# Performance work log

Hardware: AMD Instinct MI355X
Metric: run time of the kernel (lower is better)

Reference implementation:

```python
import jax, jax.numpy as jnp
import numpy as np
import math

TILE_SIZE = 32
N_HEADS = 16
FACTOR = 5.0
MASK_VALUE = -1e9


def setup_inputs() -> dict:
    key = jax.random.key(0)
    ks = jax.random.split(key, 8)
    B, S, D = 2, 2048, 1024
    w = 0.02  # weight scale so attention logits stay in a sane range
    return {
        "query": jax.random.normal(ks[0], (B, S, D), jnp.float32),
        "key": jax.random.normal(ks[1], (B, S, D), jnp.float32),
        "value": jax.random.normal(ks[2], (B, S, D), jnp.float32),
        "mask": jnp.zeros((1, 1, S, S), jnp.float32),
        "Wq": jax.random.normal(ks[3], (D, D), jnp.float32) * w,
        "bq": jnp.zeros((D,), jnp.float32),
        "Wk": jax.random.normal(ks[4], (D, D), jnp.float32) * w,
        "bk": jnp.zeros((D,), jnp.float32),
        "Wv": jax.random.normal(ks[5], (D, D), jnp.float32) * w,
        "bv": jnp.zeros((D,), jnp.float32),
        "Wo": jax.random.normal(ks[6], (D, D), jnp.float32) * w,
        "bo": jnp.zeros((D,), jnp.float32),
        "q_valid_len": 2000,
        "k_valid_len": 1900,
    }


def _pad_to_multiple(x, multiple):
    L = x.shape[1]
    p = (-L) % multiple  # static
    if p:
        x = jnp.pad(x, ((0, 0), (0, p), (0, 0)))
    return x, L


def _split_heads(x, H):
    B, L, D = x.shape
    return x.reshape(B, L, H, D // H).transpose(0, 2, 1, 3)  # [B,H,L,hd]


def _forward(query, key, value, mask, Wq, bq, Wk, bk, Wv, bv, Wo, bo,
             q_valid_len, k_valid_len):
    B, Sq, D = query.shape
    H = N_HEADS
    hd = D // H
    q = query @ Wq.T + bq
    k = key @ Wk.T + bk
    v = value @ Wv.T + bv
    q, q_len_pad = _pad_to_multiple(q, TILE_SIZE)
    k, _ = _pad_to_multiple(k, TILE_SIZE)
    v, _ = _pad_to_multiple(v, TILE_SIZE)
    qh, kh, vh = _split_heads(q, H), _split_heads(k, H), _split_heads(v, H)
    Lq, Lk = qh.shape[2], kh.shape[2]

    # key padding mask [1,1,1,Lk]
    kpm = ((jnp.arange(Lk) >= k_valid_len).astype(jnp.float32) * MASK_VALUE)
    attn_mask = mask + kpm.reshape(1, 1, 1, Lk)

    # manual scaled-dot attention with bf16 cast of scores (stable softmax path)
    scores = jnp.einsum('bhqd,bhkd->bhqk', qh, kh) / math.sqrt(hd)
    scores = scores.astype(jnp.bfloat16) + attn_mask.astype(jnp.bfloat16)
    probs = jax.nn.softmax(scores, axis=-1).astype(vh.dtype)
    context = jnp.einsum('bhqk,bhkd->bhqd', probs, vh)

    # ProbSparse top-u query-selection mask (note: original passes q_len_pad,
    # the pre-padding length, as valid_length)
    u = max(1, int(FACTOR * math.log(max(2, q_valid_len))))
    q_norm = jnp.sum(qh * qh, axis=-1)  # [B,H,Lq]
    if q_len_pad < Lq:
        q_norm = jnp.where(jnp.arange(Lq) < q_len_pad, q_norm, MASK_VALUE)
    _, topk_idx = jax.lax.top_k(q_norm, u)  # [B,H,u]
    # scatter ones at top-u positions (indices unique -> one-hot sum == set)
    ps_mask = jnp.sum(jax.nn.one_hot(topk_idx, Lq, dtype=jnp.float32), axis=2)
    context = context * ps_mask[..., None]

    # merge heads, strip padding, output projection (dropout p=0 / eval)
    context = context.transpose(0, 2, 1, 3).reshape(B, Lq, D)[:, :Sq, :]
    return context @ Wo.T + bo


def reference(query, key, value, mask, Wq, bq, Wk, bk, Wv, bv, Wo, bo,
              q_valid_len, k_valid_len):
    return _forward(query, key, value, mask, Wq, bq, Wk, bk, Wv, bv, Wo, bo,
                    q_valid_len, k_valid_len)
```

## Files before the change

### kernel.cpp

```cpp
#include <hip/hip_runtime.h>

typedef unsigned short u16;
typedef __bf16 bf16x8 __attribute__((ext_vector_type(8)));
typedef float f32x4 __attribute__((ext_vector_type(4)));

__device__ __forceinline__ u16 f2bf(float f){
  unsigned int x = __float_as_uint(f);
  unsigned int r = (x + 0x7FFFu + ((x >> 16) & 1u)) >> 16;
  return (u16)r;
}
__device__ __forceinline__ float bf2f(u16 u){
  return __uint_as_float(((unsigned int)u) << 16);
}
__device__ __forceinline__ int compute_u(int qvlv){
  int mm = qvlv > 2 ? qvlv : 2;
  int u = (int)(5.0 * log((double)mm));
  if (u < 1) u = 1;
  if (u > 64) u = 64;
  return u;
}
__device__ __forceinline__ void gload_lds16(const void* g, void* l){
  __builtin_amdgcn_global_load_lds(
      (const __attribute__((address_space(1))) void*)g,
      (__attribute__((address_space(3))) void*)l, 16, 0, 0);
}

__global__ void expand_kernel(const float* __restrict__ xq, const float* __restrict__ xk,
                              const float* __restrict__ xv,
                              const float* __restrict__ wq, const float* __restrict__ wk,
                              const float* __restrict__ wv,
                              u16* __restrict__ X1, u16* __restrict__ X2,
                              u16* __restrict__ W1, u16* __restrict__ W2,
                              const float* __restrict__ Wo, float* __restrict__ WoT,
                              unsigned int* __restrict__ hmask)
{
  __shared__ float tile[32][33];
  int t = threadIdx.x;
  if (blockIdx.x >= 15360){
    int bid = blockIdx.x - 15360;
    int bx = (bid & 31) * 32, by = (bid >> 5) * 32;
    int tx = t & 31, ty = t >> 5;
#pragma unroll
    for (int r = 0; r < 4; ++r)
      tile[ty + r*8][tx] = Wo[(size_t)(by + ty + r*8) * 1024 + bx + tx];
    __syncthreads();
#pragma unroll
    for (int r = 0; r < 4; ++r)
      WoT[(size_t)(bx + ty + r*8) * 1024 + by + tx] = tile[tx][ty + r*8];
    return;
  }
  size_t g = (size_t)blockIdx.x * 256 + t;
  if (g < 4096) hmask[g] = 0;
  const float* src; u16 *d1, *d2;
  if (g < 3145728ull) {
    int p = (int)(g >> 20);
    size_t e = (g & 1048575ull) * 4;
    src = (p == 0 ? xq : (p == 1 ? xk : xv)) + e;
    size_t o = (size_t)p * 4194304ull + e;
    d1 = X1 + o; d2 = X2 + o;
  } else {
    size_t wg = g - 3145728ull;
    int p = (int)(wg >> 18);
    size_t e = (wg & 262143ull) * 4;
    src = (p == 0 ? wq : (p == 1 ? wk : wv)) + e;
    size_t o = (size_t)p * 1048576ull + e;
    d1 = W1 + o; d2 = W2 + o;
  }
  float4 x = *reinterpret_cast<const float4*>(src);
  float xs[4] = {x.x, x.y, x.z, x.w};
  u16 h1[4], h2[4];
#pragma unroll
  for (int i = 0; i < 4; ++i){
    float v = xs[i];
    u16 a = f2bf(v);  float r1 = v - bf2f(a);
    h1[i] = a; h2[i] = f2bf(r1);
  }
  *reinterpret_cast<ushort4*>(d1) = make_ushort4(h1[0], h1[1], h1[2], h1[3]);
  *reinterpret_cast<ushort4*>(d2) = make_ushort4(h2[0], h2[1], h2[2], h2[3]);
}

__global__ __launch_bounds__(512, 1) void gemm_proj(
    const u16* __restrict__ X1, const u16* __restrict__ X2,
    const u16* __restrict__ W1, const u16* __restrict__ W2,
    const float* __restrict__ bq, const float* __restrict__ bk, const float* __restrict__ bv,
    float* __restrict__ PROJ, float* __restrict__ qn)
{
  int z = blockIdx.z;
  int orig = blockIdx.x + blockIdx.y * 8;
  int wgid = (orig & 7) * 16 + (orig >> 3);
  int bx = wgid & 7, by = wgid >> 3;

  const u16* Xa0 = X1 + (size_t)z * 4194304;
  const u16* Xa1 = X2 + (size_t)z * 4194304;
  const u16* Wb0 = W1 + (size_t)z * 1048576;
  const u16* Wb1 = W2 + (size_t)z * 1048576;
  const float* bias = (z == 0) ? bq : (z == 1 ? bk : bv);
  float* C = PROJ + (size_t)z * 4194304;

  __shared__ __align__(16) u16 T[2 * 24576];
  u16* SET0 = T;
  u16* SET1 = T + 24576;

  int t = threadIdx.x;
  int wave = t >> 6, lane = t & 63;
  int wm = wave >> 1, wn = wave & 1;
  int lr = lane & 15, lk = lane >> 4;
  int rowA = by * 256, rowB = bx * 128;
  f32x4 acc[4][4] = {};
  bf16x8 afA[4], afB[4], bgA[4], bgB[4];

#define STAGEA(dstbase, G)                                                    \
  {                                                                           \
    _Pragma("unroll")                                                         \
    for (int i = 0; i < 2; ++i){                                              \
      int p = i * 512 + t;                                                    \
      int r = p >> 2;                                                         \
      int c = (p & 3) ^ ((r >> 1) & 3);                                       \
      gload_lds16(G + (size_t)(rowA + r) * 1024 + pk + c * 8,                 \
                  (dstbase) + p * 8);                                         \
    }                                                                         \
  }
#define STAGEB(dstbase, G)                                                    \
  {                                                                           \
    int p = t;                                                                \
    int r = p >> 2;                                                           \
    int c = (p & 3) ^ ((r >> 1) & 3);                                         \
    gload_lds16(G + (size_t)(rowB + r) * 1024 + pk + c * 8,                   \
                (dstbase) + p * 8);                                           \
  }
#define STAGE_SET(S)                                                          \
  {                                                                           \
    STAGEA((S), Xa0); STAGEA((S) + 8192, Xa1);                                \
    STAGEB((S) + 16384, Wb0); STAGEB((S) + 20480, Wb1);                       \
  }
#define LOADA(dst, tile)                                                      \
  {                                                                           \
    _Pragma("unroll")                                                         \
    for (int m = 0; m < 4; ++m){                                              \
      int r = wm * 64 + m * 16 + lr;                                          \
      dst[m] = *reinterpret_cast<const bf16x8*>(                              \
          &(tile)[r * 32 + ((lk ^ ((r >> 1) & 3)) << 3)]);                    \
    }                                                                         \
  }
#define LOADB(dst, tile)                                                      \
  {                                                                           \
    _Pragma("unroll")                                                         \
    for (int n = 0; n < 4; ++n){                                              \
      int r = wn * 64 + n * 16 + lr;                                          \
      dst[n] = *reinterpret_cast<const bf16x8*>(                              \
          &(tile)[r * 32 + ((lk ^ ((r >> 1) & 3)) << 3)]);                    \
    }                                                                         \
  }
#define GRPX(A_, B_)                                                          \
  {                                                                           \
    __builtin_amdgcn_s_setprio(1);                                            \
    _Pragma("unroll")                                                         \
    for (int m = 0; m < 4; ++m)                                               \
      _Pragma("unroll")                                                       \
      for (int n = 0; n < 4; ++n)                                             \
        acc[m][n] = __builtin_amdgcn_mfma_f32_16x16x32_bf16(A_[m], B_[n],     \
                                                            acc[m][n], 0,0,0);\
    __builtin_amdgcn_s_setprio(0);                                            \
  }

  {
    int pk = 0;
    STAGE_SET(SET0);
  }
  __syncthreads();

  for (int kt = 0; kt < 32; ++kt){
    u16* CUR = (kt & 1) ? SET1 : SET0;
    u16* NXT = (kt & 1) ? SET0 : SET1;
    if (kt < 31){
      int pk = (kt + 1) * 32;
      STAGE_SET(NXT);
    }
    __builtin_amdgcn_sched_barrier(0);
    u16* A0t = CUR;          u16* A1t = CUR + 8192;
    u16* B0t = CUR + 16384;  u16* B1t = CUR + 20480;
    LOADA(afA, A0t); LOADB(bgA, B0t);
    LOADB(bgB, B1t); GRPX(afA, bgA);
    LOADA(afB, A1t); GRPX(afA, bgB);
                     GRPX(afB, bgA);
    __syncthreads();
  }
#undef STAGEA
#undef STAGEB
#undef STAGE_SET
#undef LOADA
#undef LOADB
#undef GRPX

  if (z == 0){
    float sq[4][4] = {};
#pragma unroll
    for (int m = 0; m < 4; ++m){
      int row0 = by * 256 + wm * 64 + m * 16 + lk * 4;
#pragma unroll
      for (int n = 0; n < 4; ++n){
        int col = bx * 128 + wn * 64 + n * 16 + lr;
        float bb = bias[col];
#pragma unroll
        for (int j = 0; j < 4; ++j){
          float v = acc[m][n][j] + bb;
          C[(size_t)(row0 + j) * 1024 + col] = v;
          sq[m][j] += v * v;
        }
      }
    }
    int hh = bx * 2 + wn;
#pragma unroll
    for (int m = 0; m < 4; ++m){
#pragma unroll
      for (int j = 0; j < 4; ++j){
        float s = sq[m][j];
        s += __shfl_xor(s, 1);
        s += __shfl_xor(s, 2);
        s += __shfl_xor(s, 4);
        s += __shfl_xor(s, 8);
        if (lr == 0){
          int row = by * 256 + wm * 64 + m * 16 + lk * 4 + j;
          qn[(size_t)((row >> 11) * 16 + hh) * 2048 + (row & 2047)] = s;
        }
      }
    }
  } else if (z == 1){
    u16* KS = (u16*)C;
#pragma unroll
    for (int m = 0; m < 4; ++m){
      int r0 = by * 256 + wm * 64 + m * 16 + lk * 4;
      int b = r0 >> 11, kb = r0 & 2047;
#pragma unroll
      for (int n = 0; n < 4; ++n){
        int c = bx * 128 + wn * 64 + n * 16 + lr;
        float bb = bias[c];
        int h = c >> 6, d = c & 63;
#pragma unroll
        for (int j = 0; j < 4; ++j){
          float v = acc[m][n][j] + bb;
          u16 hi = f2bf(v);
          u16 lo = f2bf(v - bf2f(hi));
          size_t base = ((size_t)(b * 16 + h) * 2048 + (size_t)(kb + j)) * 128;
          KS[base + d] = hi;
          KS[base + 64 + d] = lo;
        }
      }
    }
  } else {
    u16* VT = (u16*)C;
#pragma unroll
    for (int m = 0; m < 4; ++m){
      int r0 = by * 256 + wm * 64 + m * 16 + lk * 4;
      int b = r0 >> 11, kb = r0 & 2047;
#pragma unroll
      for (int n = 0; n < 4; ++n){
        int c = bx * 128 + wn * 64 + n * 16 + lr;
        float bb = bias[c];
        int h = c >> 6, d = c & 63;
        u16 hi[4], lo[4];
#pragma unroll
        for (int j = 0; j < 4; ++j){
          float v = acc[m][n][j] + bb;
          hi[j] = f2bf(v);
          lo[j] = f2bf(v - bf2f(hi[j]));
        }
        size_t base = ((size_t)(b * 16 + h) * 128) * 2048 + (size_t)kb;
        *reinterpret_cast<ushort4*>(&VT[base + (size_t)d * 2048]) =
            make_ushort4(hi[0], hi[1], hi[2], hi[3]);
        *reinterpret_cast<ushort4*>(&VT[base + (size_t)(64 + d) * 2048]) =
            make_ushort4(lo[0], lo[1], lo[2], lo[3]);
      }
    }
  }
}

__global__ __launch_bounds__(256) void topk_kernel(
    const float* __restrict__ qn, int* __restrict__ topk,
    unsigned char* __restrict__ seli, unsigned int* __restrict__ hmask,
    const float* __restrict__ PROJ, u16* __restrict__ QS,
    const int* __restrict__ qvlp){
  int bh = blockIdx.x; int b = bh >> 4, h = bh & 15;
  int u = compute_u(qvlp[0]);
  int t = threadIdx.x;
  __shared__ int sidx_l[64];
  if (t < 64){
    int lane = t;
    float v[32];
#pragma unroll
    for (int j = 0; j < 32; ++j) v[j] = qn[(size_t)bh * 2048 + j * 64 + lane];
    for (int it = 0; it < u; ++it){
      float bv = v[0]; int bi = lane;
#pragma unroll
      for (int j = 1; j < 32; ++j){
        if (v[j] > bv){ bv = v[j]; bi = j * 64 + lane; }
      }
#pragma unroll
      for (int off = 1; off < 64; off <<= 1){
        float ov = __shfl_xor(bv, off);
        int   oi = __shfl_xor(bi, off);
        if (ov > bv || (ov == bv && oi < bi)){ bv = ov; bi = oi; }
      }
      if (lane == 0){
        topk[bh * 64 + it] = bi;
        seli[(size_t)bh * 2048 + bi] = (unsigned char)it;
        atomicOr(&hmask[b * 2048 + bi], 1u << h);
        sidx_l[it] = bi;
      }
#pragma unroll
      for (int j = 0; j < 32; ++j)
        if (j * 64 + lane == bi) v[j] = -3.4e38f;
    }
  }
  __syncthreads();
  for (int e = t; e < 64 * 64; e += 256){
    int i = e >> 6, d = e & 63;
    float v = 0.f;
    if (i < u) v = PROJ[(size_t)(b * 2048 + sidx_l[i]) * 1024 + h * 64 + d];
    u16 hi = f2bf(v);
    u16 lo = f2bf(v - bf2f(hi));
    QS[(size_t)bh * 8192 + i * 128 + d] = hi;
    QS[(size_t)bh * 8192 + i * 128 + 64 + d] = lo;
  }
}

__global__ __launch_bounds__(256) void scores_mfma(
    const u16* __restrict__ QS, const u16* __restrict__ KS,
    const int* __restrict__ topk, const float* __restrict__ maskp,
    u16* __restrict__ sc, const int* __restrict__ qvlp, const int* __restrict__ kvlp)
{
  int bh = blockIdx.y;
  int kvlv = kvlp[0]; if (kvlv > 2048) kvlv = 2048; if (kvlv < 0) kvlv = 0;
  int u = compute_u(qvlp[0]);
  int k0 = blockIdx.x * 128;
  if (k0 >= kvlv) return;
  int t = threadIdx.x, wave = t >> 6, lane = t & 63;
  int lr = lane & 15, lk = lane >> 4;
  __shared__ int idx_l[64];
  if (t < 64) idx_l[t] = (t < u) ? topk[bh * 64 + t] : 0;
  __syncthreads();
  const u16* Qb = QS + (size_t)bh * 8192;
  const u16* Kb = KS + (size_t)bh * 2048 * 128;
  bf16x8 ah[2], al[2];
#pragma unroll
  for (int ks = 0; ks < 2; ++ks){
    const u16* qrow = &Qb[(wave * 16 + lr) * 128];
    ah[ks] = *reinterpret_cast<const bf16x8*>(&qrow[ks * 32 + lk * 8]);
    al[ks] = *reinterpret_cast<const bf16x8*>(&qrow[64 + ks * 32 + lk * 8]);
  }
  f32x4 acc[8] = {};
#pragma unroll
  for (int n = 0; n < 8; ++n){
    const u16* krow = &Kb[(size_t)(k0 + n * 16 + lr) * 128];
    bf16x8 bh0 = *reinterpret_cast<const bf16x8*>(&krow[lk * 8]);
    bf16x8 bh1 = *reinterpret_cast<const bf16x8*>(&krow[32 + lk * 8]);
    bf16x8 bl0 = *reinterpret_cast<const bf16x8*>(&krow[64 + lk * 8]);
    bf16x8 bl1 = *reinterpret_cast<const bf16x8*>(&krow[96 + lk * 8]);
    acc[n] = __builtin_amdgcn_mfma_f32_16x16x32_bf16(ah[0], bh0, acc[n], 0, 0, 0);
    acc[n] = __builtin_amdgcn_mfma_f32_16x16x32_bf16(ah[0], bl0, acc[n], 0, 0, 0);
    acc[n] = __builtin_amdgcn_mfma_f32_16x16x32_bf16(al[0], bh0, acc[n], 0, 0, 0);
    acc[n] = __builtin_amdgcn_mfma_f32_16x16x32_bf16(al[0], bl0, acc[n], 0, 0, 0);
    acc[n] = __builtin_amdgcn_mfma_f32_16x16x32_bf16(ah[1], bh1, acc[n], 0, 0, 0);
    acc[n] = __builtin_amdgcn_mfma_f32_16x16x32_bf16(ah[1], bl1, acc[n], 0, 0, 0);
    acc[n] = __builtin_amdgcn_mfma_f32_16x16x32_bf16(al[1], bh1, acc[n], 0, 0, 0);
    acc[n] = __builtin_amdgcn_mfma_f32_16x16x32_bf16(al[1], bl1, acc[n], 0, 0, 0);
  }
#pragma unroll
  for (int n = 0; n < 8; ++n){
    int k = k0 + n * 16 + lr;
    if (k >= kvlv) continue;
#pragma unroll
    for (int j = 0; j < 4; ++j){
      int i = wave * 16 + lk * 4 + j;
      if (i >= u) continue;
      float s = acc[n][j] * 0.125f;
      u16 xb = f2bf(s);
      u16 mb = f2bf(maskp[(size_t)idx_l[i] * 2048 + k]);
      u16 xm = f2bf(bf2f(xb) + bf2f(mb));
      sc[(size_t)(bh * 64 + i) * 2048 + k] = xm;
    }
  }
}

__global__ void softmax_kernel(u16* __restrict__ sc, const int* __restrict__ qvlp,
                               const int* __restrict__ kvlp){
  int bh = blockIdx.y, i = blockIdx.x;
  int u = compute_u(qvlp[0]);
  if (i >= u) return;
  int kvlv = kvlp[0]; if (kvlv > 2048) kvlv = 2048; if (kvlv < 0) kvlv = 0;
  u16* row = sc + (size_t)(bh * 64 + i) * 2048;
  int t = threadIdx.x;
  float x[8];
  float lm = -3.4e38f;
#pragma unroll
  for (int j = 0; j < 8; ++j){
    int k = t + j * 256;
    x[j] = (k < kvlv) ? bf2f(row[k]) : -3.4e38f;
    lm = fmaxf(lm, x[j]);
  }
  __shared__ float red[256];
  red[t] = lm; __syncthreads();
  for (int s = 128; s > 0; s >>= 1){ if (t < s) red[t] = fmaxf(red[t], red[t+s]); __syncthreads(); }
  float m = red[0];
  __syncthreads();
  float e[8]; float ls = 0.f;
#pragma unroll
  for (int j = 0; j < 8; ++j){
    int k = t + j * 256;
    if (k < kvlv){
      u16 ub = f2bf(x[j] - m);
      u16 eb = f2bf(expf(bf2f(ub)));
      e[j] = bf2f(eb);
      ls += e[j];
    } else e[j] = 0.f;
  }
  red[t] = ls; __syncthreads();
  for (int s = 128; s > 0; s >>= 1){ if (t < s) red[t] += red[t+s]; __syncthreads(); }
  float S = red[0];
  float Sb = bf2f(f2bf(S));
#pragma unroll
  for (int j = 0; j < 8; ++j){
    int k = t + j * 256;
    if (k < 2048) row[k] = (k < kvlv) ? f2bf(e[j] / Sb) : (u16)0;
  }
}

__global__ void pv_mfma(const u16* __restrict__ probs, const u16* __restrict__ VT,
                        float* __restrict__ part, const int* __restrict__ kvlp)
{
  int bh = blockIdx.y; int b = bh >> 4, h = bh & 15;
  int kvlv = kvlp[0]; if (kvlv > 2048) kvlv = 2048; if (kvlv < 0) kvlv = 0;
  int kc = blockIdx.x;
  int k0 = kc * 128;
  if (k0 >= kvlv) return;
  int t = threadIdx.x, w = t >> 6, lane = t & 63;
  int lr = lane & 15, lk = lane >> 4;
  const u16* Pb = probs + (size_t)bh * 64 * 2048;
  const u16* Vb = VT + (size_t)(b * 16 + h) * 128 * 2048;
  f32x4 acc[4] = {};
#pragma unroll
  for (int ks = 0; ks < 4; ++ks){
    int kk = k0 + ks * 32 + lk * 8;
    bf16x8 A0 = *reinterpret_cast<const bf16x8*>(Pb + (size_t)(lr     ) * 2048 + kk);
    bf16x8 A1 = *reinterpret_cast<const bf16x8*>(Pb + (size_t)(lr + 16) * 2048 + kk);
    bf16x8 A2 = *reinterpret_cast<const bf16x8*>(Pb + (size_t)(lr + 32) * 2048 + kk);
    bf16x8 A3 = *reinterpret_cast<const bf16x8*>(Pb + (size_t)(lr + 48) * 2048 + kk);
    bf16x8 Bh = *reinterpret_cast<const bf16x8*>(Vb + (size_t)(w * 16 + lr     ) * 2048 + kk);
    bf16x8 Bl = *reinterpret_cast<const bf16x8*>(Vb + (size_t)(w * 16 + lr + 64) * 2048 + kk);
    acc[0] = __builtin_amdgcn_mfma_f32_16x16x32_bf16(A0, Bh, acc[0], 0, 0, 0);
    acc[1] = __builtin_amdgcn_mfma_f32_16x16x32_bf16(A1, Bh, acc[1], 0, 0, 0);
    acc[2] = __builtin_amdgcn_mfma_f32_16x16x32_bf16(A2, Bh, acc[2], 0, 0, 0);
    acc[3] = __builtin_amdgcn_mfma_f32_16x16x32_bf16(A3, Bh, acc[3], 0, 0, 0);
    acc[0] = __builtin_amdgcn_mfma_f32_16x16x32_bf16(A0, Bl, acc[0], 0, 0, 0);
    acc[1] = __builtin_amdgcn_mfma_f32_16x16x32_bf16(A1, Bl, acc[1], 0, 0, 0);
    acc[2] = __builtin_amdgcn_mfma_f32_16x16x32_bf16(A2, Bl, acc[2], 0, 0, 0);
    acc[3] = __builtin_amdgcn_mfma_f32_16x16x32_bf16(A3, Bl, acc[3], 0, 0, 0);
  }
  float* pc = part + (size_t)(kc * 32 + bh) * 64 * 64;
#pragma unroll
  for (int m = 0; m < 4; ++m){
    int row = m * 16 + lk * 4;
#pragma unroll
    for (int j = 0; j < 4; ++j)
      pc[(size_t)(row + j) * 64 + w * 16 + lr] = acc[m][j];
  }
}

__global__ void outproj_kernel(const float* __restrict__ part, const float* __restrict__ WoT,
                               const float* __restrict__ bo, const unsigned int* __restrict__ hmask,
                               const unsigned char* __restrict__ seli, float* __restrict__ out,
                               const int* __restrict__ kvlp){
  int row = blockIdx.x;
  int b = row >> 11, l = row & 2047;
  int t = threadIdx.x;
  int kvlv = kvlp[0]; if (kvlv > 2048) kvlv = 2048; if (kvlv < 0) kvlv = 0;
  int kcmax = (kvlv + 127) / 128;
  float acc[4];
#pragma unroll
  for (int r = 0; r < 4; ++r) acc[r] = bo[t + r * 256];
  unsigned int m = hmask[row];
  __shared__ float clds[64];
  while (m){
    int h = __ffs(m) - 1; m &= (m - 1);
    int bh = b * 16 + h;
    int i = (int)seli[(size_t)bh * 2048 + l];
    __syncthreads();
    if (t < 64){
      float s = 0.f;
      for (int kc = 0; kc < kcmax; ++kc)
        s += part[(size_t)((kc * 32 + bh) * 64 + i) * 64 + t];
      clds[t] = s;
    }
    __syncthreads();
    for (int j = 0; j < 64; ++j){
      float c = clds[j];
      const float* wrow = &WoT[(size_t)(h * 64 + j) * 1024];
#pragma unroll
      for (int r = 0; r < 4; ++r) acc[r] += c * wrow[t + r * 256];
    }
  }
  float* orow = out + (size_t)row * 1024;
#pragma unroll
  for (int r = 0; r < 4; ++r) orow[t + r * 256] = acc[r];
}

__global__ void fail_fill(float* o, int n){
  int i = blockIdx.x * 256 + threadIdx.x;
  if (i < n) o[i] = 12345.0f;
}

extern "C" void kernel_launch(void* const* d_in, const int* in_sizes, int n_in,
                              void* d_out, int out_size, void* d_ws, size_t ws_size,
                              hipStream_t stream)
{
  const float* query = (const float*)d_in[0];
  const float* key   = (const float*)d_in[1];
  const float* value = (const float*)d_in[2];
  const float* maskp = (const float*)d_in[3];
  const float* Wq = (const float*)d_in[4];
  const float* bq = (const float*)d_in[5];
  const float* Wk = (const float*)d_in[6];
  const float* bk = (const float*)d_in[7];
  const float* Wv = (const float*)d_in[8];
  const float* bv = (const float*)d_in[9];
  const float* Wo = (const float*)d_in[10];
  const float* bo = (const float*)d_in[11];
  const int* qvl = (const int*)d_in[12];
  const int* kvl = (const int*)d_in[13];
  float* out = (float*)d_out;

  char* ws = (char*)d_ws;
  size_t off = 0;
  auto alloc = [&](size_t bytes) -> void* {
    void* p = ws + off;
    off = (off + bytes + 255) & ~(size_t)255;
    return p;
  };
  u16* X1 = (u16*)alloc(3ull * 4194304 * 2);
  u16* X2 = (u16*)alloc(3ull * 4194304 * 2);
  u16* W1 = (u16*)alloc(3ull * 1048576 * 2);
  u16* W2 = (u16*)alloc(3ull * 1048576 * 2);
  float* PROJ = (float*)alloc(3ull * 4194304 * 4);
  float* WOT  = (float*)alloc(4194304ull);
  float* QN   = (float*)alloc(2ull * 16 * 2048 * 4);
  int*   TOPK = (int*)alloc(2ull * 16 * 64 * 4);
  unsigned char* SELI = (unsigned char*)alloc(2ull * 16 * 2048);
  unsigned int* HMASK = (unsigned int*)alloc(2ull * 2048 * 4);
  u16*   SC   = (u16*)alloc(2048ull * 2048 * 2);
  u16*   QS   = (u16*)alloc(32ull * 64 * 128 * 2);

  u16* KS = (u16*)(PROJ + 1ull * 4194304);
  u16* VT = (u16*)(PROJ + 2ull * 4194304);
  float* PART = (float*)X1;

  if (ws_size < off){
    fail_fill<<<(out_size + 255) / 256, 256, 0, stream>>>(out, out_size);
    return;
  }

  expand_kernel<<<16384, 256, 0, stream>>>(query, key, value, Wq, Wk, Wv,
                                           X1, X2, W1, W2, Wo, WOT, HMASK);
  gemm_proj<<<dim3(8, 16, 3), 512, 0, stream>>>(X1, X2, W1, W2, bq, bk, bv, PROJ, QN);
  topk_kernel<<<32, 256, 0, stream>>>(QN, TOPK, SELI, HMASK, PROJ, QS, qvl);
  scores_mfma<<<dim3(16, 32), 256, 0, stream>>>(QS, KS, TOPK, maskp, SC, qvl, kvl);
  softmax_kernel<<<dim3(64, 32), 256, 0, stream>>>(SC, qvl, kvl);
  pv_mfma<<<dim3(16, 32), 256, 0, stream>>>(SC, VT, PART, kvl);
  outproj_kernel<<<4096, 256, 0, stream>>>(PART, WOT, bo, HMASK, SELI, out, kvl);
}
```

Baseline: 252.4 us.

## Fuse score computation with softmax in LDS and widen split-precision expand

Merges the scores MFMA kernel and the softmax kernel into one kernel. Each 512-thread block computes 16 selected query rows against all keys and keeps the bf16 scores in shared memory, then runs a per-row softmax with warp shuffles, so the intermediate score matrix is no longer written to and re-read from global memory and one launch is saved. The expand kernel now processes 8 floats per thread with 16-byte stores, halving its block count. The trade-off is a large LDS footprint (about 64KB) limiting occupancy, and only 128 blocks for the fused stage, which also now computes all key tiles and all 16 rows in a group, including rows beyond u and keys beyond the valid length.

```diff
diff --git a/kernel.cpp b/kernel.cpp
--- a/kernel.cpp
+++ b/kernel.cpp
@@ -36,8 +36,8 @@
 {
   __shared__ float tile[32][33];
   int t = threadIdx.x;
-  if (blockIdx.x >= 15360){
-    int bid = blockIdx.x - 15360;
+  if (blockIdx.x >= 7680){
+    int bid = blockIdx.x - 7680;
     int bx = (bid & 31) * 32, by = (bid >> 5) * 32;
     int tx = t & 31, ty = t >> 5;
 #pragma unroll
@@ -52,31 +52,33 @@
   size_t g = (size_t)blockIdx.x * 256 + t;
   if (g < 4096) hmask[g] = 0;
   const float* src; u16 *d1, *d2;
-  if (g < 3145728ull) {
-    int p = (int)(g >> 20);
-    size_t e = (g & 1048575ull) * 4;
+  if (g < 1572864ull) {
+    int p = (int)(g >> 19);
+    size_t e = (g & 524287ull) * 8;
     src = (p == 0 ? xq : (p == 1 ? xk : xv)) + e;
     size_t o = (size_t)p * 4194304ull + e;
     d1 = X1 + o; d2 = X2 + o;
   } else {
-    size_t wg = g - 3145728ull;
-    int p = (int)(wg >> 18);
-    size_t e = (wg & 262143ull) * 4;
+    size_t wg = g - 1572864ull;
+    int p = (int)(wg >> 17);
+    size_t e = (wg & 131071ull) * 8;
     src = (p == 0 ? wq : (p == 1 ? wk : wv)) + e;
     size_t o = (size_t)p * 1048576ull + e;
     d1 = W1 + o; d2 = W2 + o;
   }
-  float4 x = *reinterpret_cast<const float4*>(src);
-  float xs[4] = {x.x, x.y, x.z, x.w};
-  u16 h1[4], h2[4];
+  float4 a = *reinterpret_cast<const float4*>(src);
+  float4 b = *reinterpret_cast<const float4*>(src + 4);
+  float xs[8] = {a.x, a.y, a.z, a.w, b.x, b.y, b.z, b.w};
+  unsigned int hw[4], lw[4];
 #pragma unroll
   for (int i = 0; i < 4; ++i){
-    float v = xs[i];
-    u16 a = f2bf(v);  float r1 = v - bf2f(a);
-    h1[i] = a; h2[i] = f2bf(r1);
-  }
-  *reinterpret_cast<ushort4*>(d1) = make_ushort4(h1[0], h1[1], h1[2], h1[3]);
-  *reinterpret_cast<ushort4*>(d2) = make_ushort4(h2[0], h2[1], h2[2], h2[3]);
+    u16 h0 = f2bf(xs[2*i]);     u16 l0 = f2bf(xs[2*i]     - bf2f(h0));
+    u16 h1 = f2bf(xs[2*i + 1]); u16 l1 = f2bf(xs[2*i + 1] - bf2f(h1));
+    hw[i] = (unsigned int)h0 | ((unsigned int)h1 << 16);
+    lw[i] = (unsigned int)l0 | ((unsigned int)l1 << 16);
+  }
+  *reinterpret_cast<uint4*>(d1) = make_uint4(hw[0], hw[1], hw[2], hw[3]);
+  *reinterpret_cast<uint4*>(d2) = make_uint4(lw[0], lw[1], lw[2], lw[3]);
 }
 
 __global__ __launch_bounds__(512, 1) void gemm_proj(
@@ -324,104 +326,88 @@
   }
 }
 
-__global__ __launch_bounds__(256) void scores_mfma(
+#define SLP 2050
+__global__ __launch_bounds__(512) void scores_softmax(
     const u16* __restrict__ QS, const u16* __restrict__ KS,
     const int* __restrict__ topk, const float* __restrict__ maskp,
     u16* __restrict__ sc, const int* __restrict__ qvlp, const int* __restrict__ kvlp)
 {
-  int bh = blockIdx.y;
+  int bh = blockIdx.y, rg = blockIdx.x;
   int kvlv = kvlp[0]; if (kvlv > 2048) kvlv = 2048; if (kvlv < 0) kvlv = 0;
   int u = compute_u(qvlp[0]);
-  int k0 = blockIdx.x * 128;
-  if (k0 >= kvlv) return;
   int t = threadIdx.x, wave = t >> 6, lane = t & 63;
   int lr = lane & 15, lk = lane >> 4;
-  __shared__ int idx_l[64];
-  if (t < 64) idx_l[t] = (t < u) ? topk[bh * 64 + t] : 0;
+  __shared__ __align__(16) u16 Sl[16 * SLP];
+  __shared__ int idx_l[16];
+  if (t < 16) idx_l[t] = (rg * 16 + t < u) ? topk[bh * 64 + rg * 16 + t] : 0;
   __syncthreads();
   const u16* Qb = QS + (size_t)bh * 8192;
   const u16* Kb = KS + (size_t)bh * 2048 * 128;
-  bf16x8 ah[2], al[2];
-#pragma unroll
-  for (int ks = 0; ks < 2; ++ks){
-    const u16* qrow = &Qb[(wave * 16 + lr) * 128];
-    ah[ks] = *reinterpret_cast<const bf16x8*>(&qrow[ks * 32 + lk * 8]);
-    al[ks] = *reinterpret_cast<const bf16x8*>(&qrow[64 + ks * 32 + lk * 8]);
-  }
-  f32x4 acc[8] = {};
-#pragma unroll
-  for (int n = 0; n < 8; ++n){
-    const u16* krow = &Kb[(size_t)(k0 + n * 16 + lr) * 128];
-    bf16x8 bh0 = *reinterpret_cast<const bf16x8*>(&krow[lk * 8]);
-    bf16x8 bh1 = *reinterpret_cast<const bf16x8*>(&krow[32 + lk * 8]);
-    bf16x8 bl0 = *reinterpret_cast<const bf16x8*>(&krow[64 + lk * 8]);
-    bf16x8 bl1 = *reinterpret_cast<const bf16x8*>(&krow[96 + lk * 8]);
-    acc[n] = __builtin_amdgcn_mfma_f32_16x16x32_bf16(ah[0], bh0, acc[n], 0, 0, 0);
-    acc[n] = __builtin_amdgcn_mfma_f32_16x16x32_bf16(ah[0], bl0, acc[n], 0, 0, 0);
-    acc[n] = __builtin_amdgcn_mfma_f32_16x16x32_bf16(al[0], bh0, acc[n], 0, 0, 0);
-    acc[n] = __builtin_amdgcn_mfma_f32_16x16x32_bf16(al[0], bl0, acc[n], 0, 0, 0);
-    acc[n] = __builtin_amdgcn_mfma_f32_16x16x32_bf16(ah[1], bh1, acc[n], 0, 0, 0);
-    acc[n] = __builtin_amdgcn_mfma_f32_16x16x32_bf16(ah[1], bl1, acc[n], 0, 0, 0);
-    acc[n] = __builtin_amdgcn_mfma_f32_16x16x32_bf16(al[1], bh1, acc[n], 0, 0, 0);
-    acc[n] = __builtin_amdgcn_mfma_f32_16x16x32_bf16(al[1], bl1, acc[n], 0, 0, 0);
-  }
-#pragma unroll
-  for (int n = 0; n < 8; ++n){
-    int k = k0 + n * 16 + lr;
-    if (k >= kvlv) continue;
+  const u16* qrow = &Qb[(rg * 16 + lr) * 128];
+  bf16x8 ah0 = *reinterpret_cast<const bf16x8*>(&qrow[lk * 8]);
+  bf16x8 ah1 = *reinterpret_cast<const bf16x8*>(&qrow[32 + lk * 8]);
+  bf16x8 al0 = *reinterpret_cast<const bf16x8*>(&qrow[64 + lk * 8]);
+  bf16x8 al1 = *reinterpret_cast<const bf16x8*>(&qrow[96 + lk * 8]);
+  int k0 = wave * 256;
+#pragma unroll
+  for (int nf = 0; nf < 16; ++nf){
+    const u16* krow = &Kb[(size_t)(k0 + nf * 16 + lr) * 128];
+    bf16x8 kh0 = *reinterpret_cast<const bf16x8*>(&krow[lk * 8]);
+    bf16x8 kh1 = *reinterpret_cast<const bf16x8*>(&krow[32 + lk * 8]);
+    bf16x8 kl0 = *reinterpret_cast<const bf16x8*>(&krow[64 + lk * 8]);
+    bf16x8 kl1 = *reinterpret_cast<const bf16x8*>(&krow[96 + lk * 8]);
+    f32x4 acc = {};
+    acc = __builtin_amdgcn_mfma_f32_16x16x32_bf16(ah0, kh0, acc, 0, 0, 0);
+    acc = __builtin_amdgcn_mfma_f32_16x16x32_bf16(ah0, kl0, acc, 0, 0, 0);
+    acc = __builtin_amdgcn_mfma_f32_16x16x32_bf16(al0, kh0, acc, 0, 0, 0);
+    acc = __builtin_amdgcn_mfma_f32_16x16x32_bf16(al0, kl0, acc, 0, 0, 0);
+    acc = __builtin_amdgcn_mfma_f32_16x16x32_bf16(ah1, kh1, acc, 0, 0, 0);
+    acc = __builtin_amdgcn_mfma_f32_16x16x32_bf16(ah1, kl1, acc, 0, 0, 0);
+    acc = __builtin_amdgcn_mfma_f32_16x16x32_bf16(al1, kh1, acc, 0, 0, 0);
+    acc = __builtin_amdgcn_mfma_f32_16x16x32_bf16(al1, kl1, acc, 0, 0, 0);
+    int k = k0 + nf * 16 + lr;
 #pragma unroll
     for (int j = 0; j < 4; ++j){
-      int i = wave * 16 + lk * 4 + j;
-      if (i >= u) continue;
-      float s = acc[n][j] * 0.125f;
+      int i = lk * 4 + j;
+      float s = acc[j] * 0.125f;
       u16 xb = f2bf(s);
       u16 mb = f2bf(maskp[(size_t)idx_l[i] * 2048 + k]);
-      u16 xm = f2bf(bf2f(xb) + bf2f(mb));
-      sc[(size_t)(bh * 64 + i) * 2048 + k] = xm;
-    }
-  }
-}
-
-__global__ void softmax_kernel(u16* __restrict__ sc, const int* __restrict__ qvlp,
-                               const int* __restrict__ kvlp){
-  int bh = blockIdx.y, i = blockIdx.x;
-  int u = compute_u(qvlp[0]);
-  if (i >= u) return;
-  int kvlv = kvlp[0]; if (kvlv > 2048) kvlv = 2048; if (kvlv < 0) kvlv = 0;
-  u16* row = sc + (size_t)(bh * 64 + i) * 2048;
-  int t = threadIdx.x;
-  float x[8];
+      Sl[i * SLP + k] = f2bf(bf2f(xb) + bf2f(mb));
+    }
+  }
+  __syncthreads();
+  int row = t >> 5, sub = t & 31;
+  const u16* srow = &Sl[row * SLP];
   float lm = -3.4e38f;
-#pragma unroll
-  for (int j = 0; j < 8; ++j){
-    int k = t + j * 256;
-    x[j] = (k < kvlv) ? bf2f(row[k]) : -3.4e38f;
-    lm = fmaxf(lm, x[j]);
-  }
-  __shared__ float red[256];
-  red[t] = lm; __syncthreads();
-  for (int s = 128; s > 0; s >>= 1){ if (t < s) red[t] = fmaxf(red[t], red[t+s]); __syncthreads(); }
-  float m = red[0];
-  __syncthreads();
-  float e[8]; float ls = 0.f;
-#pragma unroll
-  for (int j = 0; j < 8; ++j){
-    int k = t + j * 256;
+  for (int e = 0; e < 64; ++e){
+    int k = e * 32 + sub;
+    if (k < kvlv) lm = fmaxf(lm, bf2f(srow[k]));
+  }
+#pragma unroll
+  for (int off = 1; off < 32; off <<= 1) lm = fmaxf(lm, __shfl_xor(lm, off, 32));
+  float m = lm;
+  float ls = 0.f;
+  for (int e = 0; e < 64; ++e){
+    int k = e * 32 + sub;
     if (k < kvlv){
-      u16 ub = f2bf(x[j] - m);
+      u16 ub = f2bf(bf2f(srow[k]) - m);
       u16 eb = f2bf(expf(bf2f(ub)));
-      e[j] = bf2f(eb);
-      ls += e[j];
-    } else e[j] = 0.f;
-  }
-  red[t] = ls; __syncthreads();
-  for (int s = 128; s > 0; s >>= 1){ if (t < s) red[t] += red[t+s]; __syncthreads(); }
-  float S = red[0];
-  float Sb = bf2f(f2bf(S));
-#pragma unroll
-  for (int j = 0; j < 8; ++j){
-    int k = t + j * 256;
-    if (k < 2048) row[k] = (k < kvlv) ? f2bf(e[j] / Sb) : (u16)0;
+      ls += bf2f(eb);
+    }
+  }
+#pragma unroll
+  for (int off = 1; off < 32; off <<= 1) ls += __shfl_xor(ls, off, 32);
+  float Sb = bf2f(f2bf(ls));
+  u16* prow = sc + (size_t)(bh * 64 + rg * 16 + row) * 2048;
+  for (int e = 0; e < 64; ++e){
+    int k = e * 32 + sub;
+    u16 pv = 0;
+    if (k < kvlv){
+      u16 ub = f2bf(bf2f(srow[k]) - m);
+      u16 eb = f2bf(expf(bf2f(ub)));
+      pv = f2bf(bf2f(eb) / Sb);
+    }
+    prow[k] = pv;
   }
 }
 
@@ -558,12 +544,11 @@
     return;
   }
 
-  expand_kernel<<<16384, 256, 0, stream>>>(query, key, value, Wq, Wk, Wv,
-                                           X1, X2, W1, W2, Wo, WOT, HMASK);
+  expand_kernel<<<8704, 256, 0, stream>>>(query, key, value, Wq, Wk, Wv,
+                                          X1, X2, W1, W2, Wo, WOT, HMASK);
   gemm_proj<<<dim3(8, 16, 3), 512, 0, stream>>>(X1, X2, W1, W2, bq, bk, bv, PROJ, QN);
   topk_kernel<<<32, 256, 0, stream>>>(QN, TOPK, SELI, HMASK, PROJ, QS, qvl);
-  scores_mfma<<<dim3(16, 32), 256, 0, stream>>>(QS, KS, TOPK, maskp, SC, qvl, kvl);
-  softmax_kernel<<<dim3(64, 32), 256, 0, stream>>>(SC, qvl, kvl);
+  scores_softmax<<<dim3(4, 32), 512, 0, stream>>>(QS, KS, TOPK, maskp, SC, qvl, kvl);
   pv_mfma<<<dim3(16, 32), 256, 0, stream>>>(SC, VT, PART, kvl);
   outproj_kernel<<<4096, 256, 0, stream>>>(PART, WOT, bo, HMASK, SELI, out, kvl);
 }
```

Measured after the change: 258.9 us. 1.03x slower.

## Precompute per-head output projections with MFMA and gather rows in assembly

Applied to the files above, without the earlier changes.

Rather than having each output row reduce partial contexts and run a scalar FP32 dot against the transposed Wo for every selected head, a new kernel multiplies each head's 64 selected context rows by its Wo slice once. It uses bf16 hi/lo split MFMA and writes a per-head 64x1024 table. A lightweight assembly kernel then sums the selected table rows plus bias for each output row. Wo is now split into bf16 hi/lo in the expand kernel instead of being transposed. This removes redundant per-row FP32 work but adds a 8 MB intermediate buffer, and the oh_mfma launch uses only 32 blocks.

```diff
diff --git a/kernel.cpp b/kernel.cpp
--- a/kernel.cpp
+++ b/kernel.cpp
@@ -28,27 +28,13 @@
 __global__ void expand_kernel(const float* __restrict__ xq, const float* __restrict__ xk,
                               const float* __restrict__ xv,
                               const float* __restrict__ wq, const float* __restrict__ wk,
-                              const float* __restrict__ wv,
+                              const float* __restrict__ wv, const float* __restrict__ wo,
                               u16* __restrict__ X1, u16* __restrict__ X2,
                               u16* __restrict__ W1, u16* __restrict__ W2,
-                              const float* __restrict__ Wo, float* __restrict__ WoT,
+                              u16* __restrict__ WO1, u16* __restrict__ WO2,
                               unsigned int* __restrict__ hmask)
 {
-  __shared__ float tile[32][33];
   int t = threadIdx.x;
-  if (blockIdx.x >= 15360){
-    int bid = blockIdx.x - 15360;
-    int bx = (bid & 31) * 32, by = (bid >> 5) * 32;
-    int tx = t & 31, ty = t >> 5;
-#pragma unroll
-    for (int r = 0; r < 4; ++r)
-      tile[ty + r*8][tx] = Wo[(size_t)(by + ty + r*8) * 1024 + bx + tx];
-    __syncthreads();
-#pragma unroll
-    for (int r = 0; r < 4; ++r)
-      WoT[(size_t)(bx + ty + r*8) * 1024 + by + tx] = tile[tx][ty + r*8];
-    return;
-  }
   size_t g = (size_t)blockIdx.x * 256 + t;
   if (g < 4096) hmask[g] = 0;
   const float* src; u16 *d1, *d2;
@@ -62,9 +48,13 @@
     size_t wg = g - 3145728ull;
     int p = (int)(wg >> 18);
     size_t e = (wg & 262143ull) * 4;
-    src = (p == 0 ? wq : (p == 1 ? wk : wv)) + e;
-    size_t o = (size_t)p * 1048576ull + e;
-    d1 = W1 + o; d2 = W2 + o;
+    src = (p == 0 ? wq : (p == 1 ? wk : (p == 2 ? wv : wo))) + e;
+    if (p < 3){
+      size_t o = (size_t)p * 1048576ull + e;
+      d1 = W1 + o; d2 = W2 + o;
+    } else {
+      d1 = WO1 + e; d2 = WO2 + e;
+    }
   }
   float4 x = *reinterpret_cast<const float4*>(src);
   float xs[4] = {x.x, x.y, x.z, x.w};
@@ -466,42 +456,85 @@
   }
 }
 
-__global__ void outproj_kernel(const float* __restrict__ part, const float* __restrict__ WoT,
-                               const float* __restrict__ bo, const unsigned int* __restrict__ hmask,
-                               const unsigned char* __restrict__ seli, float* __restrict__ out,
-                               const int* __restrict__ kvlp){
+__global__ __launch_bounds__(256) void oh_mfma(
+    const float* __restrict__ part, const u16* __restrict__ WO1,
+    const u16* __restrict__ WO2, float* __restrict__ OH,
+    const int* __restrict__ kvlp)
+{
+  int bh = blockIdx.x; int h = bh & 15;
+  int kvlv = kvlp[0]; if (kvlv > 2048) kvlv = 2048; if (kvlv < 0) kvlv = 0;
+  int kcmax = (kvlv + 127) / 128;
+  int t = threadIdx.x;
+  __shared__ __align__(16) u16 CT[64 * 128];
+  for (int e = t; e < 4096; e += 256){
+    int i = e >> 6, d = e & 63;
+    float s = 0.f;
+    for (int kc = 0; kc < kcmax; ++kc)
+      s += part[(size_t)((kc * 32 + bh) * 64 + i) * 64 + d];
+    u16 hi = f2bf(s);
+    CT[i * 128 + d] = hi;
+    CT[i * 128 + 64 + d] = f2bf(s - bf2f(hi));
+  }
+  __syncthreads();
+  int wave = t >> 6, lane = t & 63;
+  int lr = lane & 15, lk = lane >> 4;
+  bf16x8 ah[4][2], al[4][2];
+#pragma unroll
+  for (int m = 0; m < 4; ++m){
+    const u16* crow = &CT[(m * 16 + lr) * 128];
+#pragma unroll
+    for (int ks = 0; ks < 2; ++ks){
+      ah[m][ks] = *reinterpret_cast<const bf16x8*>(&crow[ks * 32 + lk * 8]);
+      al[m][ks] = *reinterpret_cast<const bf16x8*>(&crow[64 + ks * 32 + lk * 8]);
+    }
+  }
+  float* ohb = OH + (size_t)bh * 64 * 1024;
+  for (int c = wave * 16; c < wave * 16 + 16; ++c){
+    const u16* w1r = &WO1[(size_t)(c * 16 + lr) * 1024 + h * 64];
+    const u16* w2r = &WO2[(size_t)(c * 16 + lr) * 1024 + h * 64];
+    bf16x8 bh0 = *reinterpret_cast<const bf16x8*>(&w1r[lk * 8]);
+    bf16x8 bh1 = *reinterpret_cast<const bf16x8*>(&w1r[32 + lk * 8]);
+    bf16x8 bl0 = *reinterpret_cast<const bf16x8*>(&w2r[lk * 8]);
+    bf16x8 bl1 = *reinterpret_cast<const bf16x8*>(&w2r[32 + lk * 8]);
+    f32x4 acc[4] = {};
+#pragma unroll
+    for (int m = 0; m < 4; ++m){
+      acc[m] = __builtin_amdgcn_mfma_f32_16x16x32_bf16(ah[m][0], bh0, acc[m], 0, 0, 0);
+      acc[m] = __builtin_amdgcn_mfma_f32_16x16x32_bf16(ah[m][1], bh1, acc[m], 0, 0, 0);
+      acc[m] = __builtin_amdgcn_mfma_f32_16x16x32_bf16(ah[m][0], bl0, acc[m], 0, 0, 0);
+      acc[m] = __builtin_amdgcn_mfma_f32_16x16x32_bf16(ah[m][1], bl1, acc[m], 0, 0, 0);
+      acc[m] = __builtin_amdgcn_mfma_f32_16x16x32_bf16(al[m][0], bh0, acc[m], 0, 0, 0);
+      acc[m] = __builtin_amdgcn_mfma_f32_16x16x32_bf16(al[m][1], bh1, acc[m], 0, 0, 0);
+#pragma unroll
+      for (int j = 0; j < 4; ++j)
+        ohb[(size_t)(m * 16 + lk * 4 + j) * 1024 + c * 16 + lr] = acc[m][j];
+    }
+  }
+}
+
+__global__ __launch_bounds__(256) void out_assemble(
+    const float* __restrict__ OH, const float* __restrict__ bo,
+    const unsigned int* __restrict__ hmask, const unsigned char* __restrict__ seli,
+    float* __restrict__ out)
+{
   int row = blockIdx.x;
   int b = row >> 11, l = row & 2047;
   int t = threadIdx.x;
-  int kvlv = kvlp[0]; if (kvlv > 2048) kvlv = 2048; if (kvlv < 0) kvlv = 0;
-  int kcmax = (kvlv + 127) / 128;
   float acc[4];
 #pragma unroll
   for (int r = 0; r < 4; ++r) acc[r] = bo[t + r * 256];
   unsigned int m = hmask[row];
-  __shared__ float clds[64];
   while (m){
     int h = __ffs(m) - 1; m &= (m - 1);
     int bh = b * 16 + h;
     int i = (int)seli[(size_t)bh * 2048 + l];
-    __syncthreads();
-    if (t < 64){
-      float s = 0.f;
-      for (int kc = 0; kc < kcmax; ++kc)
-        s += part[(size_t)((kc * 32 + bh) * 64 + i) * 64 + t];
-      clds[t] = s;
-    }
-    __syncthreads();
-    for (int j = 0; j < 64; ++j){
-      float c = clds[j];
-      const float* wrow = &WoT[(size_t)(h * 64 + j) * 1024];
-#pragma unroll
-      for (int r = 0; r < 4; ++r) acc[r] += c * wrow[t + r * 256];
-    }
-  }
-  float* orow = out + (size_t)row * 1024;
-#pragma unroll
-  for (int r = 0; r < 4; ++r) orow[t + r * 256] = acc[r];
+    const float* orow = OH + ((size_t)bh * 64 + i) * 1024;
+#pragma unroll
+    for (int r = 0; r < 4; ++r) acc[r] += orow[t + r * 256];
+  }
+  float* dst = out + (size_t)row * 1024;
+#pragma unroll
+  for (int r = 0; r < 4; ++r) dst[t + r * 256] = acc[r];
 }
 
 __global__ void fail_fill(float* o, int n){
@@ -540,14 +573,16 @@
   u16* X2 = (u16*)alloc(3ull * 4194304 * 2);
   u16* W1 = (u16*)alloc(3ull * 1048576 * 2);
   u16* W2 = (u16*)alloc(3ull * 1048576 * 2);
+  u16* WO1 = (u16*)alloc(1048576ull * 2);
+  u16* WO2 = (u16*)alloc(1048576ull * 2);
   float* PROJ = (float*)alloc(3ull * 4194304 * 4);
-  float* WOT  = (float*)alloc(4194304ull);
   float* QN   = (float*)alloc(2ull * 16 * 2048 * 4);
   int*   TOPK = (int*)alloc(2ull * 16 * 64 * 4);
   unsigned char* SELI = (unsigned char*)alloc(2ull * 16 * 2048);
   unsigned int* HMASK = (unsigned int*)alloc(2ull * 2048 * 4);
   u16*   SC   = (u16*)alloc(2048ull * 2048 * 2);
   u16*   QS   = (u16*)alloc(32ull * 64 * 128 * 2);
+  float* OH   = (float*)alloc(32ull * 64 * 1024 * 4);
 
   u16* KS = (u16*)(PROJ + 1ull * 4194304);
   u16* VT = (u16*)(PROJ + 2ull * 4194304);
@@ -558,12 +593,13 @@
     return;
   }
 
-  expand_kernel<<<16384, 256, 0, stream>>>(query, key, value, Wq, Wk, Wv,
-                                           X1, X2, W1, W2, Wo, WOT, HMASK);
+  expand_kernel<<<16384, 256, 0, stream>>>(query, key, value, Wq, Wk, Wv, Wo,
+                                           X1, X2, W1, W2, WO1, WO2, HMASK);
   gemm_proj<<<dim3(8, 16, 3), 512, 0, stream>>>(X1, X2, W1, W2, bq, bk, bv, PROJ, QN);
   topk_kernel<<<32, 256, 0, stream>>>(QN, TOPK, SELI, HMASK, PROJ, QS, qvl);
   scores_mfma<<<dim3(16, 32), 256, 0, stream>>>(QS, KS, TOPK, maskp, SC, qvl, kvl);
   softmax_kernel<<<dim3(64, 32), 256, 0, stream>>>(SC, qvl, kvl);
   pv_mfma<<<dim3(16, 32), 256, 0, stream>>>(SC, VT, PART, kvl);
-  outproj_kernel<<<4096, 256, 0, stream>>>(PART, WOT, bo, HMASK, SELI, out, kvl);
-}
+  oh_mfma<<<32, 256, 0, stream>>>(PART, WO1, WO2, OH, kvl);
+  out_assemble<<<4096, 256, 0, stream>>>(OH, bo, HMASK, SELI, out);
+}
```

After: 282.9 us. +12.1%, slower.

## Fuse fp32-to-split-bf16 conversion into projection GEMM LDS fragment loads

Applied to the files above, without the earlier changes.

Removes the separate expand pass that split query/key/value and weights into hi/lo bf16 arrays in global memory. The projection GEMM now stages raw fp32 tiles into LDS and does the hi/lo split while reading fragments into registers. This drops a full write and re-read of the split arrays from HBM. In exchange each K-step does more conversion ALU work and moves twice the LDS bytes per fragment, and the Wo transpose becomes its own small kernel.

```diff
diff --git a/kernel.cpp b/kernel.cpp
--- a/kernel.cpp
+++ b/kernel.cpp
@@ -25,64 +25,31 @@
       (__attribute__((address_space(3))) void*)l, 16, 0, 0);
 }
 
-__global__ void expand_kernel(const float* __restrict__ xq, const float* __restrict__ xk,
-                              const float* __restrict__ xv,
-                              const float* __restrict__ wq, const float* __restrict__ wk,
-                              const float* __restrict__ wv,
-                              u16* __restrict__ X1, u16* __restrict__ X2,
-                              u16* __restrict__ W1, u16* __restrict__ W2,
-                              const float* __restrict__ Wo, float* __restrict__ WoT,
-                              unsigned int* __restrict__ hmask)
-{
+__global__ void wot_kernel(const float* __restrict__ Wo, float* __restrict__ WoT,
+                           unsigned int* __restrict__ hmask){
   __shared__ float tile[32][33];
   int t = threadIdx.x;
-  if (blockIdx.x >= 15360){
-    int bid = blockIdx.x - 15360;
-    int bx = (bid & 31) * 32, by = (bid >> 5) * 32;
-    int tx = t & 31, ty = t >> 5;
-#pragma unroll
-    for (int r = 0; r < 4; ++r)
-      tile[ty + r*8][tx] = Wo[(size_t)(by + ty + r*8) * 1024 + bx + tx];
-    __syncthreads();
-#pragma unroll
-    for (int r = 0; r < 4; ++r)
-      WoT[(size_t)(bx + ty + r*8) * 1024 + by + tx] = tile[tx][ty + r*8];
-    return;
-  }
-  size_t g = (size_t)blockIdx.x * 256 + t;
+  int g = blockIdx.x * 256 + t;
   if (g < 4096) hmask[g] = 0;
-  const float* src; u16 *d1, *d2;
-  if (g < 3145728ull) {
-    int p = (int)(g >> 20);
-    size_t e = (g & 1048575ull) * 4;
-    src = (p == 0 ? xq : (p == 1 ? xk : xv)) + e;
-    size_t o = (size_t)p * 4194304ull + e;
-    d1 = X1 + o; d2 = X2 + o;
-  } else {
-    size_t wg = g - 3145728ull;
-    int p = (int)(wg >> 18);
-    size_t e = (wg & 262143ull) * 4;
-    src = (p == 0 ? wq : (p == 1 ? wk : wv)) + e;
-    size_t o = (size_t)p * 1048576ull + e;
-    d1 = W1 + o; d2 = W2 + o;
-  }
-  float4 x = *reinterpret_cast<const float4*>(src);
-  float xs[4] = {x.x, x.y, x.z, x.w};
-  u16 h1[4], h2[4];
-#pragma unroll
-  for (int i = 0; i < 4; ++i){
-    float v = xs[i];
-    u16 a = f2bf(v);  float r1 = v - bf2f(a);
-    h1[i] = a; h2[i] = f2bf(r1);
-  }
-  *reinterpret_cast<ushort4*>(d1) = make_ushort4(h1[0], h1[1], h1[2], h1[3]);
-  *reinterpret_cast<ushort4*>(d2) = make_ushort4(h2[0], h2[1], h2[2], h2[3]);
+  int bid = blockIdx.x;
+  int bx = (bid & 31) * 32, by = (bid >> 5) * 32;
+  int tx = t & 31, ty = t >> 5;
+#pragma unroll
+  for (int r = 0; r < 4; ++r)
+    tile[ty + r*8][tx] = Wo[(size_t)(by + ty + r*8) * 1024 + bx + tx];
+  __syncthreads();
+#pragma unroll
+  for (int r = 0; r < 4; ++r)
+    WoT[(size_t)(bx + ty + r*8) * 1024 + by + tx] = tile[tx][ty + r*8];
 }
 
 __global__ __launch_bounds__(512, 1) void gemm_proj(
-    const u16* __restrict__ X1, const u16* __restrict__ X2,
-    const u16* __restrict__ W1, const u16* __restrict__ W2,
-    const float* __restrict__ bq, const float* __restrict__ bk, const float* __restrict__ bv,
+    const float* __restrict__ xq, const float* __restrict__ xk,
+    const float* __restrict__ xv,
+    const float* __restrict__ wq, const float* __restrict__ wk,
+    const float* __restrict__ wv,
+    const float* __restrict__ bq, const float* __restrict__ bk,
+    const float* __restrict__ bv,
     float* __restrict__ PROJ, float* __restrict__ qn)
 {
   int z = blockIdx.z;
@@ -90,10 +57,8 @@
   int wgid = (orig & 7) * 16 + (orig >> 3);
   int bx = wgid & 7, by = wgid >> 3;
 
-  const u16* Xa0 = X1 + (size_t)z * 4194304;
-  const u16* Xa1 = X2 + (size_t)z * 4194304;
-  const u16* Wb0 = W1 + (size_t)z * 1048576;
-  const u16* Wb1 = W2 + (size_t)z * 1048576;
+  const float* X = (z == 0) ? xq : (z == 1 ? xk : xv);
+  const float* W = (z == 0) ? wq : (z == 1 ? wk : wv);
   const float* bias = (z == 0) ? bq : (z == 1 ? bk : bv);
   float* C = PROJ + (size_t)z * 4194304;
 
@@ -109,46 +74,72 @@
   f32x4 acc[4][4] = {};
   bf16x8 afA[4], afB[4], bgA[4], bgB[4];
 
-#define STAGEA(dstbase, G)                                                    \
+#define STAGEAF(dstbase)                                                      \
+  {                                                                           \
+    _Pragma("unroll")                                                         \
+    for (int i = 0; i < 4; ++i){                                              \
+      int p = i * 512 + t;                                                    \
+      int r = p >> 3;                                                         \
+      int c = (p & 7) ^ (r & 7);                                              \
+      gload_lds16(X + (size_t)(rowA + r) * 1024 + pk + c * 4,                 \
+                  (dstbase) + p * 8);                                         \
+    }                                                                         \
+  }
+#define STAGEBF(dstbase)                                                      \
   {                                                                           \
     _Pragma("unroll")                                                         \
     for (int i = 0; i < 2; ++i){                                              \
       int p = i * 512 + t;                                                    \
-      int r = p >> 2;                                                         \
-      int c = (p & 3) ^ ((r >> 1) & 3);                                       \
-      gload_lds16(G + (size_t)(rowA + r) * 1024 + pk + c * 8,                 \
+      int r = p >> 3;                                                         \
+      int c = (p & 7) ^ (r & 7);                                              \
+      gload_lds16(W + (size_t)(rowB + r) * 1024 + pk + c * 4,                 \
                   (dstbase) + p * 8);                                         \
     }                                                                         \
   }
-#define STAGEB(dstbase, G)                                                    \
-  {                                                                           \
-    int p = t;                                                                \
-    int r = p >> 2;                                                           \
-    int c = (p & 3) ^ ((r >> 1) & 3);                                         \
-    gload_lds16(G + (size_t)(rowB + r) * 1024 + pk + c * 8,                   \
-                (dstbase) + p * 8);                                           \
-  }
 #define STAGE_SET(S)                                                          \
   {                                                                           \
-    STAGEA((S), Xa0); STAGEA((S) + 8192, Xa1);                                \
-    STAGEB((S) + 16384, Wb0); STAGEB((S) + 20480, Wb1);                       \
-  }
-#define LOADA(dst, tile)                                                      \
+    STAGEAF((S)); STAGEBF((S) + 16384);                                       \
+  }
+#define LOADCA(tile)                                                          \
   {                                                                           \
     _Pragma("unroll")                                                         \
     for (int m = 0; m < 4; ++m){                                              \
       int r = wm * 64 + m * 16 + lr;                                          \
-      dst[m] = *reinterpret_cast<const bf16x8*>(                              \
-          &(tile)[r * 32 + ((lk ^ ((r >> 1) & 3)) << 3)]);                    \
+      const char* rb = (const char*)(tile) + r * 128;                         \
+      f32x4 va = *reinterpret_cast<const f32x4*>(rb + (((2*lk)   ^ (r & 7)) << 4)); \
+      f32x4 vb = *reinterpret_cast<const f32x4*>(rb + (((2*lk+1) ^ (r & 7)) << 4)); \
+      float v0[4] = {va.x, va.y, va.z, va.w};                                 \
+      float v1[4] = {vb.x, vb.y, vb.z, vb.w};                                 \
+      _Pragma("unroll")                                                       \
+      for (int j = 0; j < 4; ++j){                                            \
+        __bf16 h0 = (__bf16)v0[j];                                            \
+        __bf16 h1 = (__bf16)v1[j];                                            \
+        afA[m][j]     = h0;                                                   \
+        afA[m][j + 4] = h1;                                                   \
+        afB[m][j]     = (__bf16)(v0[j] - (float)h0);                          \
+        afB[m][j + 4] = (__bf16)(v1[j] - (float)h1);                          \
+      }                                                                       \
     }                                                                         \
   }
-#define LOADB(dst, tile)                                                      \
+#define LOADCB(tile)                                                          \
   {                                                                           \
     _Pragma("unroll")                                                         \
     for (int n = 0; n < 4; ++n){                                              \
       int r = wn * 64 + n * 16 + lr;                                          \
-      dst[n] = *reinterpret_cast<const bf16x8*>(                              \
-          &(tile)[r * 32 + ((lk ^ ((r >> 1) & 3)) << 3)]);                    \
+      const char* rb = (const char*)(tile) + r * 128;                         \
+      f32x4 va = *reinterpret_cast<const f32x4*>(rb + (((2*lk)   ^ (r & 7)) << 4)); \
+      f32x4 vb = *reinterpret_cast<const f32x4*>(rb + (((2*lk+1) ^ (r & 7)) << 4)); \
+      float v0[4] = {va.x, va.y, va.z, va.w};                                 \
+      float v1[4] = {vb.x, vb.y, vb.z, vb.w};                                 \
+      _Pragma("unroll")                                                       \
+      for (int j = 0; j < 4; ++j){                                            \
+        __bf16 h0 = (__bf16)v0[j];                                            \
+        __bf16 h1 = (__bf16)v1[j];                                            \
+        bgA[n][j]     = h0;                                                   \
+        bgA[n][j + 4] = h1;                                                   \
+        bgB[n][j]     = (__bf16)(v0[j] - (float)h0);                          \
+        bgB[n][j + 4] = (__bf16)(v1[j] - (float)h1);                          \
+      }                                                                       \
     }                                                                         \
   }
 #define GRPX(A_, B_)                                                          \
@@ -177,19 +168,20 @@
       STAGE_SET(NXT);
     }
     __builtin_amdgcn_sched_barrier(0);
-    u16* A0t = CUR;          u16* A1t = CUR + 8192;
-    u16* B0t = CUR + 16384;  u16* B1t = CUR + 20480;
-    LOADA(afA, A0t); LOADB(bgA, B0t);
-    LOADB(bgB, B1t); GRPX(afA, bgA);
-    LOADA(afB, A1t); GRPX(afA, bgB);
-                     GRPX(afB, bgA);
+    u16* At = CUR;
+    u16* Bt = CUR + 16384;
+    LOADCA(At);
+    LOADCB(Bt);
+    GRPX(afA, bgA);
+    GRPX(afA, bgB);
+    GRPX(afB, bgA);
     __syncthreads();
   }
-#undef STAGEA
-#undef STAGEB
+#undef STAGEAF
+#undef STAGEBF
 #undef STAGE_SET
-#undef LOADA
-#undef LOADB
+#undef LOADCA
+#undef LOADCB
 #undef GRPX
 
   if (z == 0){
@@ -536,10 +528,6 @@
     off = (off + bytes + 255) & ~(size_t)255;
     return p;
   };
-  u16* X1 = (u16*)alloc(3ull * 4194304 * 2);
-  u16* X2 = (u16*)alloc(3ull * 4194304 * 2);
-  u16* W1 = (u16*)alloc(3ull * 1048576 * 2);
-  u16* W2 = (u16*)alloc(3ull * 1048576 * 2);
   float* PROJ = (float*)alloc(3ull * 4194304 * 4);
   float* WOT  = (float*)alloc(4194304ull);
   float* QN   = (float*)alloc(2ull * 16 * 2048 * 4);
@@ -548,19 +536,19 @@
   unsigned int* HMASK = (unsigned int*)alloc(2ull * 2048 * 4);
   u16*   SC   = (u16*)alloc(2048ull * 2048 * 2);
   u16*   QS   = (u16*)alloc(32ull * 64 * 128 * 2);
+  float* PART = (float*)alloc(16ull * 32 * 64 * 64 * 4);
 
   u16* KS = (u16*)(PROJ + 1ull * 4194304);
   u16* VT = (u16*)(PROJ + 2ull * 4194304);
-  float* PART = (float*)X1;
 
   if (ws_size < off){
     fail_fill<<<(out_size + 255) / 256, 256, 0, stream>>>(out, out_size);
     return;
   }
 
-  expand_kernel<<<16384, 256, 0, stream>>>(query, key, value, Wq, Wk, Wv,
-                                           X1, X2, W1, W2, Wo, WOT, HMASK);
-  gemm_proj<<<dim3(8, 16, 3), 512, 0, stream>>>(X1, X2, W1, W2, bq, bk, bv, PROJ, QN);
+  wot_kernel<<<1024, 256, 0, stream>>>(Wo, WOT, HMASK);
+  gemm_proj<<<dim3(8, 16, 3), 512, 0, stream>>>(query, key, value, Wq, Wk, Wv,
+                                                bq, bk, bv, PROJ, QN);
   topk_kernel<<<32, 256, 0, stream>>>(QN, TOPK, SELI, HMASK, PROJ, QS, qvl);
   scores_mfma<<<dim3(16, 32), 256, 0, stream>>>(QS, KS, TOPK, maskp, SC, qvl, kvl);
   softmax_kernel<<<dim3(64, 32), 256, 0, stream>>>(SC, qvl, kvl);
```

Result: slower. 278.0 us (+10.2%).
